# Performance work log

Hardware: AMD Instinct MI355X
Metric: run time of the kernel (lower is better)

## Reference

```python
import jax, jax.numpy as jnp
import numpy as np

K = 3        # kernel_size
STRIDE = 1
PAD = 1
OUT_H = 64
OUT_W = 64


def _unfold(x):
    """torch.nn.Unfold equivalent: x (B,C,H,W) -> patches (B, L, C*K*K),
    feature index ordered c*K*K + ki*K + kj (channel-major, like torch)."""
    B, C, H, W = x.shape
    xp = jnp.pad(x, ((0, 0), (0, 0), (PAD, PAD), (PAD, PAD)))
    # gather K*K shifted views; loop is over the small fixed kernel window only
    rows = []
    for ki in range(K):
        cols = []
        for kj in range(K):
            cols.append(xp[:, :, ki:ki + STRIDE * OUT_H:STRIDE,
                               kj:kj + STRIDE * OUT_W:STRIDE])  # (B,C,oh,ow)
        rows.append(jnp.stack(cols, axis=2))  # (B,C,K,oh,ow)
    p = jnp.stack(rows, axis=2)               # (B,C,K,K,oh,ow)
    # -> (B, oh, ow, C, K, K) -> (B, L, C*K*K)
    p = p.transpose(0, 4, 5, 1, 2, 3)
    return p.reshape(B, OUT_H * OUT_W, C * K * K)


def setup_inputs() -> dict:
    key = jax.random.key(0)
    k1, k2, k3 = jax.random.split(key, 3)
    B, C = 16, 32
    out_ch = 64
    L = OUT_H * OUT_W                 # 4096
    in_feat = C * K * K               # 288
    x = jax.random.normal(k1, (B, C, 64, 64), dtype=jnp.float32)
    # kaiming_uniform with a=sqrt(5) on (in_feat, out_ch) slices -> bound = 1/sqrt(in_feat)
    bound = 1.0 / np.sqrt(in_feat)
    weight = jax.random.uniform(k2, (L, in_feat, out_ch), dtype=jnp.float32,
                                minval=-bound, maxval=bound)
    bias = jax.random.uniform(k3, (L, out_ch), dtype=jnp.float32,
                              minval=-bound, maxval=bound)
    return {"x": x, "weight": weight, "bias": bias}


def reference(x, weight, bias):
    B = x.shape[0]
    out_ch = weight.shape[-1]
    patches = _unfold(x)                               # (B, L, in_feat)
    out = jnp.einsum('bli,lio->blo', patches, weight)  # per-location matmul
    out = out + bias[None]                             # (B, L, out_ch)
    out = out.transpose(0, 2, 1).reshape(B, out_ch, OUT_H, OUT_W)
    return out
```

## Files before the change

### kernel.cpp

```cpp
#include <hip/hip_runtime.h>

#define L_TOT   4096
#define CIN     32
#define G_L     4
#define CH      4
#define NCHUNK  24
#define CHUNK_STRIDE_F (CH * 3 * 64)

using f32g = __attribute__((address_space(1))) const float;
using f32l = __attribute__((address_space(3))) float;

#define FMA16(PP, WW) {                                                        \
    acc[0][0] += PP.x * WW.x; acc[0][1] += PP.x * WW.y;                        \
    acc[0][2] += PP.x * WW.z; acc[0][3] += PP.x * WW.w;                        \
    acc[1][0] += PP.y * WW.x; acc[1][1] += PP.y * WW.y;                        \
    acc[1][2] += PP.y * WW.z; acc[1][3] += PP.y * WW.w;                        \
    acc[2][0] += PP.z * WW.x; acc[2][1] += PP.z * WW.y;                        \
    acc[2][2] += PP.z * WW.z; acc[2][3] += PP.z * WW.w;                        \
    acc[3][0] += PP.w * WW.x; acc[3][1] += PP.w * WW.y;                        \
    acc[3][2] += PP.w * WW.z; acc[3][3] += PP.w * WW.w; }

#define COMPUTE4(K, WOFF) {                                                    \
    _Pragma("unroll")                                                          \
    for (int sl = 0; sl < CH; ++sl) {                                          \
        const int s = ((K) << 2) + sl;                                         \
        const float* pr = xs + ((6 * s + g) << 4) + (wv << 2);                 \
        float4 p0 = *(const float4*)(pr);                                      \
        float4 p1 = *(const float4*)(pr + 16);                                 \
        float4 p2 = *(const float4*)(pr + 32);                                 \
        const float4* wr = (const float4*)(&wsm[0][0] + (WOFF))                \
                           + g * 192 + sl * 48 + o4;                           \
        float4 w0 = wr[0];                                                     \
        float4 w1 = wr[16];                                                    \
        float4 w2 = wr[32];                                                    \
        FMA16(p0, w0); FMA16(p1, w1); FMA16(p2, w2);                           \
    } }

__global__ __launch_bounds__(256, 2)
void lc2d_v9(const float* __restrict__ x,
             const float* __restrict__ weight,
             const float* __restrict__ bias,
             float* __restrict__ out) {
    __shared__ __align__(16) float xs[576 * 16];
    __shared__ __align__(16) float wsm[3][12 * 256];

    const int tid  = threadIdx.x;
    const int lane = tid & 63;
    const int wv   = tid >> 6;
    const int g    = lane >> 4;
    const int o4   = lane & 15;

    const int bid  = blockIdx.x;
    const int swz  = ((bid & 7) << 7) | (bid >> 3);
    const int l0   = swz * G_L;
    const int oh   = l0 >> 6;
    const int ow0  = l0 & 63;

    const float* gsrc[3];
    int ldsoff[3];
#pragma unroll
    for (int t = 0; t < 3; ++t) {
        int p   = wv + (t << 2);
        int gg  = p / 3;
        int sub = p - 3 * gg;
        gsrc[t] = weight + (size_t)(l0 + gg) * (288 * 64) + sub * 256 + (lane << 2);
        ldsoff[t] = p * 256;
    }

#pragma unroll
    for (int t = 0; t < 3; ++t)
        __builtin_amdgcn_global_load_lds((f32g*)(gsrc[t]),
                                         (f32l*)(&wsm[0][ldsoff[t]]), 16, 0, 0);
#pragma unroll
    for (int t = 0; t < 3; ++t)
        __builtin_amdgcn_global_load_lds((f32g*)(gsrc[t] + CHUNK_STRIDE_F),
                                         (f32l*)(&wsm[1][ldsoff[t]]), 16, 0, 0);

    {
        const int bq = lane >> 3;
        const int w8 = lane & 7;
        const int ww = ow0 - 1 + w8;
        const bool wok = (unsigned)ww < 64u;
        const int wwc = wok ? ww : 0;
#pragma unroll 8
        for (int j = 0; j < 48; ++j) {
            int task  = (j << 2) + wv;
            int bhalf = task & 1;
            int t     = task >> 1;
            int c     = t / 3;
            int dh    = t - 3 * c;
            int h     = oh - 1 + dh;
            bool hok  = (unsigned)h < 64u;
            int hc    = hok ? h : 0;
            float v = x[((size_t)((bhalf << 3) + bq) << 17)
                        + (((c << 6) + hc) << 6) + wwc];
            v = (hok && wok) ? v : 0.0f;
            if (w8 < 6)
                xs[(t * 6 + w8) * 16 + (bhalf << 3) + bq] = v;
        }
    }
    __syncthreads();

    const float4 bias4 = ((const float4*)bias)[(l0 + g) * 16 + o4];
    float acc[4][4];
#pragma unroll
    for (int bq = 0; bq < 4; ++bq) {
        acc[bq][0] = bias4.x; acc[bq][1] = bias4.y;
        acc[bq][2] = bias4.z; acc[bq][3] = bias4.w;
    }

    int wo0 = 0;
    int wo1 = 12 * 256;
    int wo2 = 2 * 12 * 256;
    for (int k = 0; k < NCHUNK - 2; ++k) {
#pragma unroll
        for (int t = 0; t < 3; ++t)
            __builtin_amdgcn_global_load_lds(
                (f32g*)(gsrc[t] + (size_t)(k + 2) * CHUNK_STRIDE_F),
                (f32l*)(&wsm[0][0] + wo2 + ldsoff[t]), 16, 0, 0);
        COMPUTE4(k, wo0);
        asm volatile("s_waitcnt vmcnt(3) lgkmcnt(0)" ::: "memory");
        __builtin_amdgcn_s_barrier();
        asm volatile("" ::: "memory");
        int tmp = wo0; wo0 = wo1; wo1 = wo2; wo2 = tmp;
    }
    COMPUTE4(NCHUNK - 2, wo0);
    asm volatile("s_waitcnt vmcnt(0) lgkmcnt(0)" ::: "memory");
    __builtin_amdgcn_s_barrier();
    asm volatile("" ::: "memory");
    COMPUTE4(NCHUNK - 1, wo1);

#pragma unroll
    for (int bq = 0; bq < 4; ++bq) {
        const int b = (wv << 2) + bq;
#pragma unroll
        for (int j = 0; j < 4; ++j) {
            out[((size_t)((b << 6) + (o4 << 2) + j) << 12) + l0 + g] = acc[bq][j];
        }
    }
}

extern "C" void kernel_launch(void* const* d_in, const int* in_sizes, int n_in,
                              void* d_out, int out_size, void* d_ws, size_t ws_size,
                              hipStream_t stream) {
    const float* x      = (const float*)d_in[0];
    const float* weight = (const float*)d_in[1];
    const float* bias   = (const float*)d_in[2];
    float* out          = (float*)d_out;

    dim3 grid(L_TOT / G_L);
    dim3 block(256);
    hipLaunchKernelGGL(lc2d_v9, grid, block, 0, stream, x, weight, bias, out);
}
```

Baseline: 426.8 us.

## Replace direct-to-LDS weight loads with register-staged triple prefetch and double-buffered LDS

Weight chunks are now fetched into registers three chunks ahead and written to LDS one step before use. This replaces the global_load_lds triple-buffered LDS scheme with two LDS buffers. The aim is more memory requests in flight and less LDS use, and the bias load and first weight loads are hoisted above the input staging. The cost is extra VGPRs for three float4x3 staging sets and explicit LDS store instructions, which may hurt occupancy under the 2-block launch bound.

```diff
diff --git a/kernel.cpp b/kernel.cpp
--- a/kernel.cpp
+++ b/kernel.cpp
@@ -5,10 +5,7 @@
 #define G_L     4
 #define CH      4
 #define NCHUNK  24
-#define CHUNK_STRIDE_F (CH * 3 * 64)
-
-using f32g = __attribute__((address_space(1))) const float;
-using f32l = __attribute__((address_space(3))) float;
+#define CSF     (CH * 3 * 64)
 
 #define FMA16(PP, WW) {                                                        \
     acc[0][0] += PP.x * WW.x; acc[0][1] += PP.x * WW.y;                        \
@@ -20,7 +17,7 @@
     acc[3][0] += PP.w * WW.x; acc[3][1] += PP.w * WW.y;                        \
     acc[3][2] += PP.w * WW.z; acc[3][3] += PP.w * WW.w; }
 
-#define COMPUTE4(K, WOFF) {                                                    \
+#define COMPUTE4(K, BI) {                                                      \
     _Pragma("unroll")                                                          \
     for (int sl = 0; sl < CH; ++sl) {                                          \
         const int s = ((K) << 2) + sl;                                         \
@@ -28,21 +25,32 @@
         float4 p0 = *(const float4*)(pr);                                      \
         float4 p1 = *(const float4*)(pr + 16);                                 \
         float4 p2 = *(const float4*)(pr + 32);                                 \
-        const float4* wr = (const float4*)(&wsm[0][0] + (WOFF))                \
-                           + g * 192 + sl * 48 + o4;                           \
+        const float4* wr = (const float4*)&wsm[BI][0] + g * 192 + sl * 48 + o4;\
         float4 w0 = wr[0];                                                     \
         float4 w1 = wr[16];                                                    \
         float4 w2 = wr[32];                                                    \
         FMA16(p0, w0); FMA16(p1, w1); FMA16(p2, w2);                           \
     } }
 
+#define ISSUE(SL, K) { _Pragma("unroll") for (int t = 0; t < 3; ++t)           \
+    SL[t] = *(const float4*)(gsrc[t] + (size_t)(K) * CSF); }
+
+#define PUBLISH(SL, BI) { _Pragma("unroll") for (int t = 0; t < 3; ++t)        \
+    *(float4*)(&wsm[BI][ldsoff[t] + (lane << 2)]) = SL[t]; }
+
+#define FENCE_BAR() { asm volatile("s_waitcnt lgkmcnt(0)" ::: "memory");       \
+    __builtin_amdgcn_s_barrier(); }
+
+#define BODY(J, SISS, SPUB) { ISSUE(SISS, (J) + 3); COMPUTE4((J), (J) & 1);    \
+    PUBLISH(SPUB, ((J) + 1) & 1); FENCE_BAR(); }
+
 __global__ __launch_bounds__(256, 2)
-void lc2d_v9(const float* __restrict__ x,
-             const float* __restrict__ weight,
-             const float* __restrict__ bias,
-             float* __restrict__ out) {
+void lc2d_v10(const float* __restrict__ x,
+              const float* __restrict__ weight,
+              const float* __restrict__ bias,
+              float* __restrict__ out) {
     __shared__ __align__(16) float xs[576 * 16];
-    __shared__ __align__(16) float wsm[3][12 * 256];
+    __shared__ __align__(16) float wsm[2][12 * 256];
 
     const int tid  = threadIdx.x;
     const int lane = tid & 63;
@@ -67,14 +75,13 @@
         ldsoff[t] = p * 256;
     }
 
-#pragma unroll
-    for (int t = 0; t < 3; ++t)
-        __builtin_amdgcn_global_load_lds((f32g*)(gsrc[t]),
-                                         (f32l*)(&wsm[0][ldsoff[t]]), 16, 0, 0);
-#pragma unroll
-    for (int t = 0; t < 3; ++t)
-        __builtin_amdgcn_global_load_lds((f32g*)(gsrc[t] + CHUNK_STRIDE_F),
-                                         (f32l*)(&wsm[1][ldsoff[t]]), 16, 0, 0);
+    const float4 bias4 = ((const float4*)bias)[(l0 + g) * 16 + o4];
+
+    float4 sA[3], sB[3], sC[3];
+
+    ISSUE(sA, 0);
+    ISSUE(sB, 1);
+    ISSUE(sC, 2);
 
     {
         const int bq = lane >> 3;
@@ -83,8 +90,8 @@
         const bool wok = (unsigned)ww < 64u;
         const int wwc = wok ? ww : 0;
 #pragma unroll 8
-        for (int j = 0; j < 48; ++j) {
-            int task  = (j << 2) + wv;
+        for (int jj = 0; jj < 48; ++jj) {
+            int task  = (jj << 2) + wv;
             int bhalf = task & 1;
             int t     = task >> 1;
             int c     = t / 3;
@@ -99,9 +106,7 @@
                 xs[(t * 6 + w8) * 16 + (bhalf << 3) + bq] = v;
         }
     }
-    __syncthreads();
 
-    const float4 bias4 = ((const float4*)bias)[(l0 + g) * 16 + o4];
     float acc[4][4];
 #pragma unroll
     for (int bq = 0; bq < 4; ++bq) {
@@ -109,26 +114,17 @@
         acc[bq][2] = bias4.z; acc[bq][3] = bias4.w;
     }
 
-    int wo0 = 0;
-    int wo1 = 12 * 256;
-    int wo2 = 2 * 12 * 256;
-    for (int k = 0; k < NCHUNK - 2; ++k) {
-#pragma unroll
-        for (int t = 0; t < 3; ++t)
-            __builtin_amdgcn_global_load_lds(
-                (f32g*)(gsrc[t] + (size_t)(k + 2) * CHUNK_STRIDE_F),
-                (f32l*)(&wsm[0][0] + wo2 + ldsoff[t]), 16, 0, 0);
-        COMPUTE4(k, wo0);
-        asm volatile("s_waitcnt vmcnt(3) lgkmcnt(0)" ::: "memory");
-        __builtin_amdgcn_s_barrier();
-        asm volatile("" ::: "memory");
-        int tmp = wo0; wo0 = wo1; wo1 = wo2; wo2 = tmp;
+    PUBLISH(sA, 0);
+    FENCE_BAR();
+
+    for (int j = 0; j <= 18; j += 3) {
+        BODY(j + 0, sA, sB);
+        BODY(j + 1, sB, sC);
+        BODY(j + 2, sC, sA);
     }
-    COMPUTE4(NCHUNK - 2, wo0);
-    asm volatile("s_waitcnt vmcnt(0) lgkmcnt(0)" ::: "memory");
-    __builtin_amdgcn_s_barrier();
-    asm volatile("" ::: "memory");
-    COMPUTE4(NCHUNK - 1, wo1);
+    COMPUTE4(21, 1); PUBLISH(sB, 0); FENCE_BAR();
+    COMPUTE4(22, 0); PUBLISH(sC, 1); FENCE_BAR();
+    COMPUTE4(23, 1);
 
 #pragma unroll
     for (int bq = 0; bq < 4; ++bq) {
@@ -150,5 +146,5 @@
 
     dim3 grid(L_TOT / G_L);
     dim3 block(256);
-    hipLaunchKernelGGL(lc2d_v9, grid, block, 0, stream, x, weight, bias, out);
+    hipLaunchKernelGGL(lc2d_v10, grid, block, 0, stream, x, weight, bias, out);
 }
```

Result: slower. 439.1 us (+2.9%).
